# Optimization experiments

Hardware: AMD Instinct MI355X
Metric: run time of the kernel (lower is better)

## Reference

```python
import jax, jax.numpy as jnp
import numpy as np

ALPHA = 16
M_FACTORS = [8, 16, 8]
N_FACTORS = [8, 16, 8]


def setup_inputs() -> dict:
    key = jax.random.key(0)
    ks = jax.random.split(key, 9)
    B, S, D = 8, 2048, 1024
    r = 8
    x = jax.random.normal(ks[0], (B, S, D), dtype=jnp.float32)
    W = jax.random.normal(ks[1], (D, D), dtype=jnp.float32) * 0.02
    b = jax.random.normal(ks[2], (D,), dtype=jnp.float32) * 0.02
    # m-cores: (r_prev, m_i, r_next), first rank = 1
    core0 = jax.random.normal(ks[3], (1, 8, r), dtype=jnp.float32) * 0.1
    core1 = jax.random.normal(ks[4], (r, 16, r), dtype=jnp.float32) * 0.1
    core2 = jax.random.normal(ks[5], (r, 8, r), dtype=jnp.float32) * 0.1
    # n-cores: (r_prev, n_i, r_next), last rank = 1
    core3 = jax.random.normal(ks[6], (r, 8, r), dtype=jnp.float32) * 0.1
    core4 = jax.random.normal(ks[7], (r, 16, r), dtype=jnp.float32) * 0.1
    core5 = jax.random.normal(ks[8], (r, 8, 1), dtype=jnp.float32) * 0.1
    return {"x": x, "W": W, "b": b, "core0": core0, "core1": core1,
            "core2": core2, "core3": core3, "core4": core4, "core5": core5}


def tensorized_multiplication(x, m_cores, n_cores, m_factors):
    B, S, _ = x.shape
    # [B, 1, S, m_k, ..., m_1] : input dim split into m_factors, reversed
    tt = x.reshape((B, S) + tuple(m_factors[::-1]))[:, None]
    for core in m_cores:
        # contract trailing m-factor and current rank, new rank at axis 1
        tt = jnp.einsum('br...m,rmp->bp...', tt, core)
    for core in n_cores:
        # expand n-factor at the end, carry rank at axis 1
        tt = jnp.einsum('br...,rnp->bp...n', tt, core)
    # tt: [B, 1, S, n_1, ..., n_k] -> [B, S, prod(n_factors)]
    return tt.reshape(B, S, -1)


def reference(x, W, b, core0, core1, core2, core3, core4, core5):
    z = tensorized_multiplication(x, [core0, core1, core2],
                                  [core3, core4, core5], M_FACTORS)
    base = jnp.einsum('bsd,od->bso', x, W) + b  # nn.Linear: x @ W.T + b
    return base + z * ALPHA
```

## Files before the change

### kernel.cpp

```cpp
#include <hip/hip_runtime.h>
#include <hip/hip_bf16.h>


#define D_DIM 1024
#define BS_ROWS 16384
#define ALPHA_F 16.0f
#define BM 128
#define BN 128

using bf16   = __bf16;
using bf16x8 = __attribute__((ext_vector_type(8))) __bf16;
using bf16x4 = __attribute__((ext_vector_type(4))) __bf16;
using f32x4  = __attribute__((ext_vector_type(4))) float;

#define GPTR(p) (const __attribute__((address_space(1))) void*)(p)
#define SPTR(p) (__attribute__((address_space(3))) void*)(p)

__global__ __launch_bounds__(256) void prep_kernel(
    const float* __restrict__ X,
    const float* __restrict__ W,
    const float* __restrict__ c0, const float* __restrict__ c1,
    const float* __restrict__ c2, const float* __restrict__ c3,
    const float* __restrict__ c4, const float* __restrict__ c5,
    bf16* __restrict__ Weff, bf16* __restrict__ Xb)
{
    __shared__ float t2[1024];
    __shared__ float Msh[8192];
    const int tid = threadIdx.x;

    if (blockIdx.x >= 1024) {
        size_t i = ((size_t)(blockIdx.x - 1024) * 256 + tid) * 8;
        f32x4 a = *(const f32x4*)&X[i];
        f32x4 b = *(const f32x4*)&X[i + 4];
        bf16x8 v;
        v[0] = (bf16)a[0]; v[1] = (bf16)a[1]; v[2] = (bf16)a[2]; v[3] = (bf16)a[3];
        v[4] = (bf16)b[0]; v[5] = (bf16)b[1]; v[6] = (bf16)b[2]; v[7] = (bf16)b[3];
        *(bf16x8*)&Xb[i] = v;
        return;
    }

    const int o = blockIdx.x;
    for (int e = tid; e < 1024; e += 256) {
        int p2 = e & 7, i2i1 = e >> 3;
        int i1 = i2i1 & 7, i2 = i2i1 >> 3;
        float s = 0.f;
        for (int p1 = 0; p1 < 8; ++p1)
            s += c0[i1 * 8 + p1] * c1[p1 * 128 + i2 * 8 + p2];
        t2[e] = s;
    }
    __syncthreads();
    for (int e = tid; e < 8192; e += 256) {
        int p3 = e & 7, d = e >> 3;
        int i1 = d & 7, i2 = (d >> 3) & 15, i3 = d >> 7;
        float s = 0.f;
        for (int p2 = 0; p2 < 8; ++p2)
            s += t2[(i2 * 8 + i1) * 8 + p2] * c2[p2 * 64 + i3 * 8 + p3];
        Msh[e] = s;
    }

    int n1 = o >> 7, nn = o & 127, n2 = nn >> 3, n3 = nn & 7;
    float v[8];
    for (int p4 = 0; p4 < 8; ++p4) {
        float s = 0.f;
        for (int p5 = 0; p5 < 8; ++p5)
            s += c4[p4 * 128 + n2 * 8 + p5] * c5[p5 * 8 + n3];
        v[p4] = s;
    }
    float ncol[8];
    for (int r3 = 0; r3 < 8; ++r3) {
        float s = 0.f;
        for (int p4 = 0; p4 < 8; ++p4)
            s += c3[r3 * 64 + n1 * 8 + p4] * v[p4];
        ncol[r3] = s;
    }
    __syncthreads();

    int d0 = tid * 4;
    f32x4 w = *(const f32x4*)&W[o * D_DIM + d0];
    bf16x4 res;
    for (int k = 0; k < 4; ++k) {
        float acc = 0.f;
        for (int r = 0; r < 8; ++r)
            acc += Msh[(d0 + k) * 8 + r] * ncol[r];
        res[k] = (bf16)(w[k] + ALPHA_F * acc);
    }
    *(bf16x4*)&Weff[o * D_DIM + d0] = res;
}

__global__ __launch_bounds__(256) void gemm_bb_kernel(
    const bf16* __restrict__ Xb,
    const bf16* __restrict__ Weff,
    const float* __restrict__ bias,
    float* __restrict__ Out)
{
    __shared__ __align__(16) bf16 As[BM][64];
    __shared__ __align__(16) bf16 Bs[BN][64];

    const int tid  = threadIdx.x;
    const int wave = tid >> 6, lane = tid & 63;
    const int mtile = blockIdx.x, ntile = blockIdx.y;
    const int wr = wave >> 1, wc = wave & 1;
    const int l15 = lane & 15, quad = lane >> 4;

    const int srow = wave * 32 + (lane >> 3);
    const int gchunk = (lane & 7) ^ (lane >> 3);
    const bf16* asrc = Xb   + (size_t)(mtile * BM + srow) * D_DIM + gchunk * 8;
    const bf16* bsrc = Weff + (size_t)(ntile * BN + srow) * D_DIM + gchunk * 8;
    char* abase = (char*)&As[0][0] + wave * 4096;
    char* bbase = (char*)&Bs[0][0] + wave * 4096;

    const int rsw = l15 & 7;

    f32x4 acc[4][4];
    for (int i = 0; i < 4; ++i)
        for (int j = 0; j < 4; ++j)
            for (int r = 0; r < 4; ++r) acc[i][j][r] = 0.f;

    for (int kt = 0; kt < D_DIM / 64; ++kt) {
        const int ko = kt * 64;
        for (int j = 0; j < 4; ++j) {
            __builtin_amdgcn_global_load_lds(GPTR(asrc + (size_t)j * 8 * D_DIM + ko),
                                             SPTR(abase + j * 1024), 16, 0, 0);
            __builtin_amdgcn_global_load_lds(GPTR(bsrc + (size_t)j * 8 * D_DIM + ko),
                                             SPTR(bbase + j * 1024), 16, 0, 0);
        }

        __syncthreads();

        for (int kk = 0; kk < 2; ++kk) {
            const int lc = kk * 4 + quad;
            const int sc = (lc ^ rsw) * 8;
            bf16x8 af[4], bfr[4];
            for (int i = 0; i < 4; ++i)
                af[i] = *(const bf16x8*)&As[wr * 64 + i * 16 + l15][sc];
            for (int j = 0; j < 4; ++j)
                bfr[j] = *(const bf16x8*)&Bs[wc * 64 + j * 16 + l15][sc];
            for (int i = 0; i < 4; ++i)
                for (int j = 0; j < 4; ++j)
                    acc[i][j] = __builtin_amdgcn_mfma_f32_16x16x32_bf16(
                        af[i], bfr[j], acc[i][j], 0, 0, 0);
        }

        __syncthreads();
    }

    float bj[4];
    for (int j = 0; j < 4; ++j)
        bj[j] = bias[ntile * BN + wc * 64 + j * 16 + l15];
    for (int i = 0; i < 4; ++i) {
        int row0 = mtile * BM + wr * 64 + i * 16 + quad * 4;
        for (int r = 0; r < 4; ++r) {
            float* orow = Out + (size_t)(row0 + r) * D_DIM + ntile * BN + wc * 64 + l15;
            for (int j = 0; j < 4; ++j)
                orow[j * 16] = acc[i][j][r] + bj[j];
        }
    }
}

__global__ __launch_bounds__(256) void gemm_bias_kernel(
    const float* __restrict__ X,
    const bf16* __restrict__ Weff,
    const float* __restrict__ bias,
    float* __restrict__ Out)
{
    __shared__ __align__(16) bf16 As[BM][32];
    __shared__ __align__(16) bf16 Bs[BN][32];

    const int tid  = threadIdx.x;
    const int wave = tid >> 6, lane = tid & 63;
    const int mtile = blockIdx.x, ntile = blockIdx.y;
    const int wr = wave >> 1, wc = wave & 1;
    const int l15 = lane & 15, quad = lane >> 4;

    const int ar = tid >> 1, ah = tid & 1;
    const float* xsrc = X + (size_t)(mtile * BM + ar) * D_DIM + ah * 16;
    bf16* adst = &As[ar][ah * 16];

    const bf16* bsrc0 = Weff + (size_t)(ntile * BN + wave * 32 + (lane >> 2)) * D_DIM
                        + (lane & 3) * 8;
    const bf16* bsrc1 = bsrc0 + 16 * D_DIM;
    char* bbase = (char*)&Bs[0][0];
    void* bdst0 = bbase + wave * 2048;
    void* bdst1 = bbase + wave * 2048 + 1024;

    f32x4 acc[4][4];
    for (int i = 0; i < 4; ++i)
        for (int j = 0; j < 4; ++j)
            for (int r = 0; r < 4; ++r) acc[i][j][r] = 0.f;

    for (int kt = 0; kt < D_DIM / 32; ++kt) {
        __builtin_amdgcn_global_load_lds(GPTR(bsrc0 + kt * 32), SPTR(bdst0), 16, 0, 0);
        __builtin_amdgcn_global_load_lds(GPTR(bsrc1 + kt * 32), SPTR(bdst1), 16, 0, 0);

        const f32x4* xp = (const f32x4*)(xsrc + kt * 32);
        f32x4 f0 = xp[0], f1 = xp[1], f2 = xp[2], f3 = xp[3];
        bf16x8 p0, p1;
        p0[0] = (bf16)f0[0]; p0[1] = (bf16)f0[1]; p0[2] = (bf16)f0[2]; p0[3] = (bf16)f0[3];
        p0[4] = (bf16)f1[0]; p0[5] = (bf16)f1[1]; p0[6] = (bf16)f1[2]; p0[7] = (bf16)f1[3];
        p1[0] = (bf16)f2[0]; p1[1] = (bf16)f2[1]; p1[2] = (bf16)f2[2]; p1[3] = (bf16)f2[3];
        p1[4] = (bf16)f3[0]; p1[5] = (bf16)f3[1]; p1[6] = (bf16)f3[2]; p1[7] = (bf16)f3[3];
        *(bf16x8*)adst = p0;
        *(bf16x8*)(adst + 8) = p1;

        __syncthreads();

        bf16x8 af[4], bfr[4];
        for (int i = 0; i < 4; ++i)
            af[i] = *(const bf16x8*)&As[wr * 64 + i * 16 + l15][quad * 8];
        for (int j = 0; j < 4; ++j)
            bfr[j] = *(const bf16x8*)&Bs[wc * 64 + j * 16 + l15][quad * 8];
        for (int i = 0; i < 4; ++i)
            for (int j = 0; j < 4; ++j)
                acc[i][j] = __builtin_amdgcn_mfma_f32_16x16x32_bf16(
                    af[i], bfr[j], acc[i][j], 0, 0, 0);

        __syncthreads();
    }

    float bj[4];
    for (int j = 0; j < 4; ++j)
        bj[j] = bias[ntile * BN + wc * 64 + j * 16 + l15];
    for (int i = 0; i < 4; ++i) {
        int row0 = mtile * BM + wr * 64 + i * 16 + quad * 4;
        for (int r = 0; r < 4; ++r) {
            float* orow = Out + (size_t)(row0 + r) * D_DIM + ntile * BN + wc * 64 + l15;
            for (int j = 0; j < 4; ++j)
                orow[j * 16] = acc[i][j][r] + bj[j];
        }
    }
}

__global__ __launch_bounds__(256) void build_weff_fused_kernel(
    const float* __restrict__ W,
    const float* __restrict__ c0, const float* __restrict__ c1,
    const float* __restrict__ c2, const float* __restrict__ c3,
    const float* __restrict__ c4, const float* __restrict__ c5,
    bf16* __restrict__ Weff)
{
    __shared__ float t2[1024];
    __shared__ float Msh[8192];
    const int tid = threadIdx.x;
    const int o = blockIdx.x;

    for (int e = tid; e < 1024; e += 256) {
        int p2 = e & 7, i2i1 = e >> 3;
        int i1 = i2i1 & 7, i2 = i2i1 >> 3;
        float s = 0.f;
        for (int p1 = 0; p1 < 8; ++p1)
            s += c0[i1 * 8 + p1] * c1[p1 * 128 + i2 * 8 + p2];
        t2[e] = s;
    }
    __syncthreads();
    for (int e = tid; e < 8192; e += 256) {
        int p3 = e & 7, d = e >> 3;
        int i1 = d & 7, i2 = (d >> 3) & 15, i3 = d >> 7;
        float s = 0.f;
        for (int p2 = 0; p2 < 8; ++p2)
            s += t2[(i2 * 8 + i1) * 8 + p2] * c2[p2 * 64 + i3 * 8 + p3];
        Msh[e] = s;
    }
    int n1 = o >> 7, nn = o & 127, n2 = nn >> 3, n3 = nn & 7;
    float v[8];
    for (int p4 = 0; p4 < 8; ++p4) {
        float s = 0.f;
        for (int p5 = 0; p5 < 8; ++p5)
            s += c4[p4 * 128 + n2 * 8 + p5] * c5[p5 * 8 + n3];
        v[p4] = s;
    }
    float ncol[8];
    for (int r3 = 0; r3 < 8; ++r3) {
        float s = 0.f;
        for (int p4 = 0; p4 < 8; ++p4)
            s += c3[r3 * 64 + n1 * 8 + p4] * v[p4];
        ncol[r3] = s;
    }
    __syncthreads();

    int d0 = tid * 4;
    f32x4 w = *(const f32x4*)&W[o * D_DIM + d0];
    bf16x4 res;
    for (int k = 0; k < 4; ++k) {
        float acc = 0.f;
        for (int r = 0; r < 8; ++r)
            acc += Msh[(d0 + k) * 8 + r] * ncol[r];
        res[k] = (bf16)(w[k] + ALPHA_F * acc);
    }
    *(bf16x4*)&Weff[o * D_DIM + d0] = res;
}

extern "C" void kernel_launch(void* const* d_in, const int* in_sizes, int n_in,
                              void* d_out, int out_size, void* d_ws, size_t ws_size,
                              hipStream_t stream) {
    const float* x  = (const float*)d_in[0];
    const float* W  = (const float*)d_in[1];
    const float* b  = (const float*)d_in[2];
    const float* c0 = (const float*)d_in[3];
    const float* c1 = (const float*)d_in[4];
    const float* c2 = (const float*)d_in[5];
    const float* c3 = (const float*)d_in[6];
    const float* c4 = (const float*)d_in[7];
    const float* c5 = (const float*)d_in[8];
    float* out = (float*)d_out;

    char* ws = (char*)d_ws;
    bf16* Weff = (bf16*)ws;
    bf16* Xb   = (bf16*)(ws + 4u * 1024u * 1024u);
    const size_t need = 4u * 1024u * 1024u + (size_t)BS_ROWS * D_DIM * 2u;

    dim3 grid(BS_ROWS / BM, D_DIM / BN);
    if (ws_size >= need) {
        prep_kernel<<<1024 + 8192, 256, 0, stream>>>(x, W, c0, c1, c2, c3, c4, c5,
                                                     Weff, Xb);
        gemm_bb_kernel<<<grid, 256, 0, stream>>>(Xb, Weff, b, out);
    } else {
        build_weff_fused_kernel<<<D_DIM, 256, 0, stream>>>(W, c0, c1, c2, c3, c4, c5, Weff);
        gemm_bias_kernel<<<grid, 256, 0, stream>>>(x, Weff, b, out);
    }
}
```

Measured before the change: 184.6 us.

## Add triple-buffered 256x128 bf16 GEMM with direct global-to-LDS loads

```diff
diff --git a/kernel.cpp b/kernel.cpp
--- a/kernel.cpp
+++ b/kernel.cpp
@@ -85,6 +85,128 @@
         res[k] = (bf16)(w[k] + ALPHA_F * acc);
     }
     *(bf16x4*)&Weff[o * D_DIM + d0] = res;
+}
+
+#define TBM 256
+#define TBN 128
+#define ABYTES (TBM * 128)
+#define BBYTES (TBN * 128)
+#define BUFB   (ABYTES + BBYTES)
+#define NBUFS  3
+#define NTILES (D_DIM / 64)
+
+__global__ __launch_bounds__(512, 2) void gemm_pipe_kernel(
+    const bf16* __restrict__ Xb,
+    const bf16* __restrict__ Weff,
+    const float* __restrict__ bias,
+    float* __restrict__ Out)
+{
+    extern __shared__ __attribute__((aligned(16))) char smem[];
+
+    const int tid  = threadIdx.x;
+    const int wave = tid >> 6, lane = tid & 63;
+
+    const int bid   = blockIdx.x;
+    const int slot  = (bid & 7) * 64 + (bid >> 3);
+    const int mtile = slot >> 3;
+    const int ntile = slot & 7;
+
+    const int wr = wave >> 1, wc = wave & 1;
+    const int l15 = lane & 15, quad = lane >> 4;
+    const int rsw = l15 & 7;
+
+    const int srow   = wave * 8 + (lane >> 3);
+    const int gchunk = (lane & 7) ^ (lane >> 3);
+    const bf16* asrc = Xb   + (size_t)(mtile * TBM + srow) * D_DIM + gchunk * 8;
+    const bf16* bsrc = Weff + (size_t)(ntile * TBN + srow) * D_DIM + gchunk * 8;
+    const int woff = wave * 1024;
+
+    auto STAGE = [&](int bo, int t) {
+        const bf16* ap = asrc + t * 64;
+        const bf16* bp = bsrc + t * 64;
+        char* ad = smem + bo + woff;
+        char* bd = smem + bo + ABYTES + woff;
+#pragma unroll
+        for (int j = 0; j < 4; ++j)
+            __builtin_amdgcn_global_load_lds(GPTR(ap + (size_t)j * 64 * D_DIM),
+                                             SPTR(ad + j * 8192), 16, 0, 0);
+#pragma unroll
+        for (int j = 0; j < 2; ++j)
+            __builtin_amdgcn_global_load_lds(GPTR(bp + (size_t)j * 64 * D_DIM),
+                                             SPTR(bd + j * 8192), 16, 0, 0);
+    };
+
+    f32x4 acc[4][4];
+#pragma unroll
+    for (int i = 0; i < 4; ++i)
+#pragma unroll
+        for (int j = 0; j < 4; ++j)
+#pragma unroll
+            for (int r = 0; r < 4; ++r) acc[i][j][r] = 0.f;
+
+    auto COMPUTE = [&](int bo) {
+        const bf16* Ab = (const bf16*)(smem + bo);
+        const bf16* Bb = (const bf16*)(smem + bo + ABYTES);
+#pragma unroll
+        for (int kk = 0; kk < 2; ++kk) {
+            const int sc = ((kk * 4 + quad) ^ rsw) * 8;
+            bf16x8 af[4], bfr[4];
+#pragma unroll
+            for (int i = 0; i < 4; ++i)
+                af[i] = *(const bf16x8*)&Ab[(wr * 64 + i * 16 + l15) * 64 + sc];
+#pragma unroll
+            for (int j = 0; j < 4; ++j)
+                bfr[j] = *(const bf16x8*)&Bb[(wc * 64 + j * 16 + l15) * 64 + sc];
+            __builtin_amdgcn_s_setprio(1);
+#pragma unroll
+            for (int i = 0; i < 4; ++i)
+#pragma unroll
+                for (int j = 0; j < 4; ++j)
+                    acc[i][j] = __builtin_amdgcn_mfma_f32_16x16x32_bf16(
+                        af[i], bfr[j], acc[i][j], 0, 0, 0);
+            __builtin_amdgcn_s_setprio(0);
+        }
+    };
+
+    STAGE(0, 0);
+    STAGE(BUFB, 1);
+    asm volatile("s_waitcnt vmcnt(6)" ::: "memory");
+    __builtin_amdgcn_s_barrier();
+    __builtin_amdgcn_sched_barrier(0);
+
+    int bo = 0;
+#pragma unroll
+    for (int t = 0; t < NTILES - 2; ++t) {
+        int bs = bo + 2 * BUFB; if (bs >= NBUFS * BUFB) bs -= NBUFS * BUFB;
+        STAGE(bs, t + 2);
+        COMPUTE(bo);
+        asm volatile("s_waitcnt vmcnt(6) lgkmcnt(0)" ::: "memory");
+        __builtin_amdgcn_s_barrier();
+        __builtin_amdgcn_sched_barrier(0);
+        bo += BUFB; if (bo == NBUFS * BUFB) bo = 0;
+    }
+    COMPUTE(bo);
+    asm volatile("s_waitcnt vmcnt(0) lgkmcnt(0)" ::: "memory");
+    __builtin_amdgcn_s_barrier();
+    __builtin_amdgcn_sched_barrier(0);
+    bo += BUFB; if (bo == NBUFS * BUFB) bo = 0;
+    COMPUTE(bo);
+
+    float bj[4];
+#pragma unroll
+    for (int j = 0; j < 4; ++j)
+        bj[j] = bias[ntile * TBN + wc * 64 + j * 16 + l15];
+#pragma unroll
+    for (int i = 0; i < 4; ++i) {
+        int row0 = mtile * TBM + wr * 64 + i * 16 + quad * 4;
+#pragma unroll
+        for (int r = 0; r < 4; ++r) {
+            float* orow = Out + (size_t)(row0 + r) * D_DIM + ntile * TBN + wc * 64 + l15;
+#pragma unroll
+            for (int j = 0; j < 4; ++j)
+                orow[j * 16] = acc[i][j][r] + bj[j];
+        }
+    }
 }
 
 __global__ __launch_bounds__(256) void gemm_bb_kernel(
@@ -307,13 +429,26 @@
     bf16* Xb   = (bf16*)(ws + 4u * 1024u * 1024u);
     const size_t need = 4u * 1024u * 1024u + (size_t)BS_ROWS * D_DIM * 2u;
 
-    dim3 grid(BS_ROWS / BM, D_DIM / BN);
+    static int smem_ok = -1;
+    if (smem_ok < 0) {
+        hipError_t e = hipFuncSetAttribute((const void*)gemm_pipe_kernel,
+                                           hipFuncAttributeMaxDynamicSharedMemorySize,
+                                           NBUFS * BUFB);
+        smem_ok = (e == hipSuccess) ? 1 : 0;
+    }
+
     if (ws_size >= need) {
         prep_kernel<<<1024 + 8192, 256, 0, stream>>>(x, W, c0, c1, c2, c3, c4, c5,
                                                      Weff, Xb);
-        gemm_bb_kernel<<<grid, 256, 0, stream>>>(Xb, Weff, b, out);
+        if (smem_ok) {
+            gemm_pipe_kernel<<<dim3(512), 512, NBUFS * BUFB, stream>>>(Xb, Weff, b, out);
+        } else {
+            dim3 grid(BS_ROWS / BM, D_DIM / BN);
+            gemm_bb_kernel<<<grid, 256, 0, stream>>>(Xb, Weff, b, out);
+        }
     } else {
         build_weff_fused_kernel<<<D_DIM, 256, 0, stream>>>(W, c0, c1, c2, c3, c4, c5, Weff);
+        dim3 grid(BS_ROWS / BM, D_DIM / BN);
         gemm_bias_kernel<<<grid, 256, 0, stream>>>(x, Weff, b, out);
     }
 }
```

After: 175.3 us. -5.0%, faster.
